# Kernel optimization log

Measured on AMD Instinct MI355X. Metric: run time of the kernel, lower is better.

Reference implementation:

```python
import math
import jax, jax.numpy as jnp
import numpy as np

NUM_HEADS = 8

def setup_inputs() -> dict:
    key = jax.random.key(0)
    ks = jax.random.split(key, 4)
    b, c, T, H, W = 8, 512, 8, 16, 16
    data_dim = T * H * W  # 2048
    x = jax.random.normal(ks[0], (b, c, T, H, W), dtype=jnp.float32)
    pos_emb = jax.random.normal(ks[1], (c, data_dim + 1), dtype=jnp.float32) / math.sqrt(c)
    w_qkv = jax.random.normal(ks[2], (3 * c, c), dtype=jnp.float32) * (1.0 / math.sqrt(c))
    b_qkv = jnp.zeros((3 * c,), dtype=jnp.float32)
    w_c = jax.random.normal(ks[3], (c, c), dtype=jnp.float32) * (1.0 / math.sqrt(c))
    b_c = jnp.zeros((c,), dtype=jnp.float32)
    return {"x": x, "pos_emb": pos_emb, "w_qkv": w_qkv, "b_qkv": b_qkv, "w_c": w_c, "b_c": b_c}

def reference(x, pos_emb, w_qkv, b_qkv, w_c, b_c):
    b, c = x.shape[0], x.shape[1]
    xf = x.reshape(b, c, -1)                                   # [b, c, THW]
    xf = jnp.concatenate([xf.mean(axis=-1, keepdims=True), xf], axis=-1)  # [b, c, T+1]
    xf = xf + pos_emb[None].astype(xf.dtype)
    qkv = jnp.einsum('oc,bct->bot', w_qkv, xf) + b_qkv[None, :, None]      # [b, 3c, L]
    L = qkv.shape[-1]
    ch = c // NUM_HEADS
    q, k, v = jnp.split(qkv, 3, axis=1)
    q = q.reshape(b * NUM_HEADS, ch, L)
    k = k.reshape(b * NUM_HEADS, ch, L)
    v = v.reshape(b * NUM_HEADS, ch, L)
    scale = 1.0 / math.sqrt(math.sqrt(ch))
    w = jnp.einsum('bct,bcs->bts', q * scale, k * scale)        # [bH, L, L]
    w = jax.nn.softmax(w.astype(jnp.float32), axis=-1).astype(qkv.dtype)
    a = jnp.einsum('bts,bcs->bct', w, v).reshape(b, c, L)       # [b, c, L]
    out = jnp.einsum('oc,bct->bot', w_c, a) + b_c[None, :, None]
    return out[:, :, 0]                                         # [b, out_dim]
```

## Files before the change

### kernel.cpp

```cpp
#include <hip/hip_runtime.h>

#define B 8
#define C 512
#define D 2048
#define L 2049
#define NH 8
#define CH 64
#define NLT 32
#define TLD 513

__device__ __forceinline__ float wave_sum(float v) {
  #pragma unroll
  for (int off = 32; off; off >>= 1) v += __shfl_down(v, off);
  return v;
}
__device__ __forceinline__ float wave_max(float v) {
  #pragma unroll
  for (int off = 32; off; off >>= 1) v = fmaxf(v, __shfl_down(v, off));
  return v;
}
__device__ __forceinline__ float lane_bcast(float v, int l) {
  return __uint_as_float(__builtin_amdgcn_readlane(__float_as_uint(v), l));
}

__global__ void __launch_bounds__(256) k_mean(const float* __restrict__ x, float* __restrict__ mean) {
  int row = blockIdx.x;
  const float4* xr = reinterpret_cast<const float4*>(x + (size_t)row * D);
  float s = 0.f;
  #pragma unroll
  for (int i = 0; i < 2; ++i) {
    float4 v = xr[threadIdx.x + i * 256];
    s += (v.x + v.y) + (v.z + v.w);
  }
  __shared__ float red[4];
  s = wave_sum(s);
  if ((threadIdx.x & 63) == 0) red[threadIdx.x >> 6] = s;
  __syncthreads();
  if (threadIdx.x == 0) mean[row] = (red[0] + red[1] + red[2] + red[3]) * (1.0f / D);
}

__global__ void __launch_bounds__(256) k_qu(const float* __restrict__ wqkv,
                                            const float* __restrict__ bqkv,
                                            const float* __restrict__ pos,
                                            const float* __restrict__ mean,
                                            float* __restrict__ u,
                                            float* __restrict__ logit0,
                                            float* __restrict__ mps_g) {
  int bh = blockIdx.x, b = bh >> 3, h = bh & 7;
  int tid = threadIdx.x, wid = tid >> 6, lane = tid & 63;
  __shared__ float mps[C];
  __shared__ float q0s[CH];
  __shared__ float us[C];
  __shared__ float red[4];
  for (int c = tid; c < C; c += 256) {
    float v = mean[b * C + c] + pos[(size_t)c * L];
    mps[c] = v;
    if (h == 0) mps_g[b * C + c] = v;
  }
  __syncthreads();
  for (int j = wid; j < CH; j += 4) {
    const float* wr = wqkv + (size_t)(h * CH + j) * C;
    float acc = 0.f;
    #pragma unroll
    for (int k = 0; k < 8; ++k) acc += wr[lane + k * 64] * mps[lane + k * 64];
    acc = wave_sum(acc);
    if (lane == 0) q0s[j] = acc + bqkv[h * CH + j];
  }
  __syncthreads();
  float a0 = 0.f, a1 = 0.f;
  #pragma unroll 4
  for (int j = 0; j < CH; ++j) {
    float qv = q0s[j];
    const float* wkr = wqkv + (size_t)(C + h * CH + j) * C;
    a0 += qv * wkr[tid];
    a1 += qv * wkr[tid + 256];
  }
  a0 *= 0.125f; a1 *= 0.125f;
  us[tid] = a0; us[tid + 256] = a1;
  u[(size_t)bh * C + tid] = a0;
  u[(size_t)bh * C + tid + 256] = a1;
  __syncthreads();
  float p = us[tid] * mps[tid] + us[tid + 256] * mps[tid + 256];
  p = wave_sum(p);
  if (lane == 0) red[wid] = p;
  __syncthreads();
  if (tid == 0) logit0[bh] = red[0] + red[1] + red[2] + red[3];
}

__global__ void __launch_bounds__(512, 1) k_fused_lx(
    const float* __restrict__ x, const float* __restrict__ pos,
    const float* __restrict__ u_g,
    float* __restrict__ xpart, float* __restrict__ mpart, float* __restrict__ spart) {
  __shared__ float tile[64][TLD];
  __shared__ float rlds[8][NH][64];
  __shared__ float e_t[64][9];
  int lt = blockIdx.x, b = blockIdx.y;
  int tid = threadIdx.x, wid = tid >> 6, lane = tid & 63;
  int cg = wid * 64;
  int col = lt * 64 + lane;

  float ureg[NH];
  #pragma unroll
  for (int h = 0; h < NH; ++h) ureg[h] = u_g[(size_t)(b * NH + h) * C + cg + lane];

  float acc[NH];
  #pragma unroll
  for (int h = 0; h < NH; ++h) acc[h] = 0.f;

  const float* xp = x + ((size_t)(b * C + cg)) * D + col;
  const float* pp = pos + (size_t)cg * L + col + 1;
  #pragma unroll
  for (int cc = 0; cc < 64; ++cc) {
    float v = xp[(size_t)cc * D] + pp[(size_t)cc * L];
    tile[lane][cg + cc] = v;
    #pragma unroll
    for (int h = 0; h < NH; ++h) acc[h] += lane_bcast(ureg[h], cc) * v;
  }
  #pragma unroll
  for (int h = 0; h < NH; ++h) rlds[wid][h][lane] = acc[h];
  __syncthreads();

  {
    int h = wid;
    float lg = 0.f;
    #pragma unroll
    for (int w = 0; w < 8; ++w) lg += rlds[w][h][lane];
    float m = wave_max(lg);
    m = lane_bcast(m, 0);
    float e = __expf(lg - m);
    float s = wave_sum(e);
    e_t[lane][h] = e;
    if (lane == 0) {
      mpart[(b * NH + h) * NLT + lt] = m;
      spart[(b * NH + h) * NLT + lt] = s;
    }
  }
  __syncthreads();

  float epre[NH];
  #pragma unroll
  for (int h = 0; h < NH; ++h) epre[h] = e_t[lane][h];
  float a2[NH];
  #pragma unroll
  for (int h = 0; h < NH; ++h) a2[h] = 0.f;
  #pragma unroll
  for (int l = 0; l < 64; ++l) {
    float xv = tile[l][tid];
    #pragma unroll
    for (int h = 0; h < NH; ++h) a2[h] += lane_bcast(epre[h], l) * xv;
  }
  #pragma unroll
  for (int h = 0; h < NH; ++h)
    xpart[(((size_t)b * NLT + lt) * NH + h) * C + tid] = a2[h];
}

__global__ void __launch_bounds__(512) k_a0(
    const float* __restrict__ xpart, const float* __restrict__ mpart,
    const float* __restrict__ spart, const float* __restrict__ logit0,
    const float* __restrict__ mps_g,
    const float* __restrict__ wqkv, const float* __restrict__ bqkv,
    float* __restrict__ a0v) {
  int bh = blockIdx.x, b = bh >> 3, h = bh & 7;
  int tid = threadIdx.x, wid = tid >> 6, lane = tid & 63;
  __shared__ float row[C];
  float lg0 = logit0[bh];
  float mt = (lane < NLT) ? mpart[bh * NLT + lane] : -3.0e38f;
  float M = fmaxf(lane_bcast(wave_max(mt), 0), lg0);
  float rr = (lane < NLT) ? __expf(mt - M) : 0.f;
  float st = (lane < NLT) ? spart[bh * NLT + lane] * rr : 0.f;
  float S = lane_bcast(wave_sum(st), 0) + __expf(lg0 - M);
  float Sinv = 1.0f / S;
  float acc = 0.f;
  #pragma unroll
  for (int t = 0; t < NLT; ++t)
    acc += xpart[(((size_t)b * NLT + t) * NH + h) * C + tid] * lane_bcast(rr, t);
  acc = (acc + __expf(lg0 - M) * mps_g[b * C + tid]) * Sinv;
  row[tid] = acc;
  __syncthreads();
  float xr[8];
  #pragma unroll
  for (int k = 0; k < 8; ++k) xr[k] = row[k * 64 + lane];
  #pragma unroll 2
  for (int j = 0; j < 8; ++j) {
    int o = h * CH + wid * 8 + j;
    const float* wr = wqkv + (size_t)(2 * C + o) * C;
    float d = 0.f;
    #pragma unroll
    for (int k = 0; k < 8; ++k) d += wr[k * 64 + lane] * xr[k];
    d = wave_sum(d);
    if (lane == 0) a0v[b * C + o] = d + bqkv[2 * C + o];
  }
}

__global__ void __launch_bounds__(512) k_out(const float* __restrict__ wc,
                                             const float* __restrict__ bc,
                                             const float* __restrict__ a0v,
                                             float* __restrict__ out) {
  int bid = blockIdx.x, b = bid >> 3, og = (bid & 7) * 64;
  int tid = threadIdx.x, wid = tid >> 6, lane = tid & 63;
  __shared__ float row[C];
  row[tid] = a0v[b * C + tid];
  __syncthreads();
  float xr[8];
  #pragma unroll
  for (int k = 0; k < 8; ++k) xr[k] = row[k * 64 + lane];
  #pragma unroll 2
  for (int j = 0; j < 8; ++j) {
    int o = og + wid * 8 + j;
    const float* wr = wc + (size_t)o * C;
    float d = 0.f;
    #pragma unroll
    for (int k = 0; k < 8; ++k) d += wr[k * 64 + lane] * xr[k];
    d = wave_sum(d);
    if (lane == 0) out[b * C + o] = d + bc[o];
  }
}

extern "C" void kernel_launch(void* const* d_in, const int* in_sizes, int n_in,
                              void* d_out, int out_size, void* d_ws, size_t ws_size,
                              hipStream_t stream) {
  const float* x    = (const float*)d_in[0];
  const float* pos  = (const float*)d_in[1];
  const float* wqkv = (const float*)d_in[2];
  const float* bqkv = (const float*)d_in[3];
  const float* wc   = (const float*)d_in[4];
  const float* bc   = (const float*)d_in[5];
  float* out = (float*)d_out;
  float* ws  = (float*)d_ws;

  float* mean   = ws;
  float* u      = ws + 4096;
  float* logit0 = ws + 36864;
  float* mpart  = ws + 36928;
  float* spart  = ws + 38976;
  float* a0v    = ws + 41024;
  float* mps_g  = ws + 45120;
  float* xpart  = ws + 49216;

  hipLaunchKernelGGL(k_mean,     dim3(B * C),    dim3(256), 0, stream, x, mean);
  hipLaunchKernelGGL(k_qu,       dim3(B * NH),   dim3(256), 0, stream, wqkv, bqkv, pos, mean, u, logit0, mps_g);
  hipLaunchKernelGGL(k_fused_lx, dim3(NLT, B),   dim3(512), 0, stream, x, pos, u, xpart, mpart, spart);
  hipLaunchKernelGGL(k_a0,       dim3(B * NH),   dim3(512), 0, stream, xpart, mpart, spart, logit0,
                     mps_g, wqkv, bqkv, a0v);
  hipLaunchKernelGGL(k_out,      dim3(B * NH),   dim3(512), 0, stream, wc, bc, a0v, out);
}
```

Before: 56.03 us.

## Fuse value and output projections into one tail kernel and batch loads in main kernel

Folds the pos-embedding add into the mean kernel, and merges the softmax combine, value projection and output projection into a single per-batch tail kernel, removing one launch and an intermediate buffer. In the main fused kernel, all 64 x and pos loads are issued up front into a register array, and the second phase reads the LDS tile in batches of 32, to expose more memory-level parallelism. Launch bounds are raised to allow two blocks per CU. The tail kernel runs only 8 blocks and streams both weight matrices serially per block, so it may become latency-bound, and the large register arrays under a tighter register budget risk spills.

```diff
diff --git a/kernel.cpp b/kernel.cpp
--- a/kernel.cpp
+++ b/kernel.cpp
@@ -23,7 +23,9 @@
   return __uint_as_float(__builtin_amdgcn_readlane(__float_as_uint(v), l));
 }
 
-__global__ void __launch_bounds__(256) k_mean(const float* __restrict__ x, float* __restrict__ mean) {
+__global__ void __launch_bounds__(256) k_mean(const float* __restrict__ x,
+                                              const float* __restrict__ pos,
+                                              float* __restrict__ mps_g) {
   int row = blockIdx.x;
   const float4* xr = reinterpret_cast<const float4*>(x + (size_t)row * D);
   float s = 0.f;
@@ -36,27 +38,23 @@
   s = wave_sum(s);
   if ((threadIdx.x & 63) == 0) red[threadIdx.x >> 6] = s;
   __syncthreads();
-  if (threadIdx.x == 0) mean[row] = (red[0] + red[1] + red[2] + red[3]) * (1.0f / D);
+  if (threadIdx.x == 0)
+    mps_g[row] = (red[0] + red[1] + red[2] + red[3]) * (1.0f / D)
+               + pos[(size_t)(row & (C - 1)) * L];
 }
 
 __global__ void __launch_bounds__(256) k_qu(const float* __restrict__ wqkv,
                                             const float* __restrict__ bqkv,
-                                            const float* __restrict__ pos,
-                                            const float* __restrict__ mean,
+                                            const float* __restrict__ mps_g,
                                             float* __restrict__ u,
-                                            float* __restrict__ logit0,
-                                            float* __restrict__ mps_g) {
+                                            float* __restrict__ logit0) {
   int bh = blockIdx.x, b = bh >> 3, h = bh & 7;
   int tid = threadIdx.x, wid = tid >> 6, lane = tid & 63;
   __shared__ float mps[C];
   __shared__ float q0s[CH];
   __shared__ float us[C];
   __shared__ float red[4];
-  for (int c = tid; c < C; c += 256) {
-    float v = mean[b * C + c] + pos[(size_t)c * L];
-    mps[c] = v;
-    if (h == 0) mps_g[b * C + c] = v;
-  }
+  for (int c = tid; c < C; c += 256) mps[c] = mps_g[b * C + c];
   __syncthreads();
   for (int j = wid; j < CH; j += 4) {
     const float* wr = wqkv + (size_t)(h * CH + j) * C;
@@ -87,7 +85,7 @@
   if (tid == 0) logit0[bh] = red[0] + red[1] + red[2] + red[3];
 }
 
-__global__ void __launch_bounds__(512, 1) k_fused_lx(
+__global__ void __launch_bounds__(512, 2) k_fused_lx(
     const float* __restrict__ x, const float* __restrict__ pos,
     const float* __restrict__ u_g,
     float* __restrict__ xpart, float* __restrict__ mpart, float* __restrict__ spart) {
@@ -103,18 +101,23 @@
   #pragma unroll
   for (int h = 0; h < NH; ++h) ureg[h] = u_g[(size_t)(b * NH + h) * C + cg + lane];
 
-  float acc[NH];
-  #pragma unroll
-  for (int h = 0; h < NH; ++h) acc[h] = 0.f;
-
   const float* xp = x + ((size_t)(b * C + cg)) * D + col;
   const float* pp = pos + (size_t)cg * L + col + 1;
+
+  float v_arr[64];
+  #pragma unroll
+  for (int cc = 0; cc < 64; ++cc) v_arr[cc] = xp[(size_t)cc * D];
+  #pragma unroll
+  for (int cc = 0; cc < 64; ++cc) v_arr[cc] += pp[(size_t)cc * L];
+
+  float acc[NH];
+  #pragma unroll
+  for (int h = 0; h < NH; ++h) acc[h] = 0.f;
   #pragma unroll
   for (int cc = 0; cc < 64; ++cc) {
-    float v = xp[(size_t)cc * D] + pp[(size_t)cc * L];
-    tile[lane][cg + cc] = v;
-    #pragma unroll
-    for (int h = 0; h < NH; ++h) acc[h] += lane_bcast(ureg[h], cc) * v;
+    tile[lane][cg + cc] = v_arr[cc];
+    #pragma unroll
+    for (int h = 0; h < NH; ++h) acc[h] += lane_bcast(ureg[h], cc) * v_arr[cc];
   }
   #pragma unroll
   for (int h = 0; h < NH; ++h) rlds[wid][h][lane] = acc[h];
@@ -144,75 +147,85 @@
   #pragma unroll
   for (int h = 0; h < NH; ++h) a2[h] = 0.f;
   #pragma unroll
-  for (int l = 0; l < 64; ++l) {
-    float xv = tile[l][tid];
-    #pragma unroll
-    for (int h = 0; h < NH; ++h) a2[h] += lane_bcast(epre[h], l) * xv;
+  for (int half = 0; half < 2; ++half) {
+    float xv[32];
+    #pragma unroll
+    for (int i = 0; i < 32; ++i) xv[i] = tile[half * 32 + i][tid];
+    #pragma unroll
+    for (int i = 0; i < 32; ++i) {
+      #pragma unroll
+      for (int h = 0; h < NH; ++h)
+        a2[h] += lane_bcast(epre[h], half * 32 + i) * xv[i];
+    }
   }
   #pragma unroll
   for (int h = 0; h < NH; ++h)
     xpart[(((size_t)b * NLT + lt) * NH + h) * C + tid] = a2[h];
 }
 
-__global__ void __launch_bounds__(512) k_a0(
+__global__ void __launch_bounds__(512) k_tail(
     const float* __restrict__ xpart, const float* __restrict__ mpart,
     const float* __restrict__ spart, const float* __restrict__ logit0,
     const float* __restrict__ mps_g,
     const float* __restrict__ wqkv, const float* __restrict__ bqkv,
-    float* __restrict__ a0v) {
-  int bh = blockIdx.x, b = bh >> 3, h = bh & 7;
+    const float* __restrict__ wc, const float* __restrict__ bc,
+    float* __restrict__ out) {
+  int b = blockIdx.x;
   int tid = threadIdx.x, wid = tid >> 6, lane = tid & 63;
-  __shared__ float row[C];
-  float lg0 = logit0[bh];
-  float mt = (lane < NLT) ? mpart[bh * NLT + lane] : -3.0e38f;
-  float M = fmaxf(lane_bcast(wave_max(mt), 0), lg0);
-  float rr = (lane < NLT) ? __expf(mt - M) : 0.f;
-  float st = (lane < NLT) ? spart[bh * NLT + lane] * rr : 0.f;
-  float S = lane_bcast(wave_sum(st), 0) + __expf(lg0 - M);
-  float Sinv = 1.0f / S;
-  float acc = 0.f;
-  #pragma unroll
-  for (int t = 0; t < NLT; ++t)
-    acc += xpart[(((size_t)b * NLT + t) * NH + h) * C + tid] * lane_bcast(rr, t);
-  acc = (acc + __expf(lg0 - M) * mps_g[b * C + tid]) * Sinv;
-  row[tid] = acc;
-  __syncthreads();
-  float xr[8];
-  #pragma unroll
-  for (int k = 0; k < 8; ++k) xr[k] = row[k * 64 + lane];
-  #pragma unroll 2
-  for (int j = 0; j < 8; ++j) {
-    int o = h * CH + wid * 8 + j;
-    const float* wr = wqkv + (size_t)(2 * C + o) * C;
-    float d = 0.f;
-    #pragma unroll
-    for (int k = 0; k < 8; ++k) d += wr[k * 64 + lane] * xr[k];
-    d = wave_sum(d);
-    if (lane == 0) a0v[b * C + o] = d + bqkv[2 * C + o];
-  }
-}
-
-__global__ void __launch_bounds__(512) k_out(const float* __restrict__ wc,
-                                             const float* __restrict__ bc,
-                                             const float* __restrict__ a0v,
-                                             float* __restrict__ out) {
-  int bid = blockIdx.x, b = bid >> 3, og = (bid & 7) * 64;
-  int tid = threadIdx.x, wid = tid >> 6, lane = tid & 63;
-  __shared__ float row[C];
-  row[tid] = a0v[b * C + tid];
-  __syncthreads();
-  float xr[8];
-  #pragma unroll
-  for (int k = 0; k < 8; ++k) xr[k] = row[k * 64 + lane];
-  #pragma unroll 2
-  for (int j = 0; j < 8; ++j) {
-    int o = og + wid * 8 + j;
-    const float* wr = wc + (size_t)o * C;
-    float d = 0.f;
-    #pragma unroll
-    for (int k = 0; k < 8; ++k) d += wr[k * 64 + lane] * xr[k];
-    d = wave_sum(d);
-    if (lane == 0) out[b * C + o] = d + bc[o];
+  __shared__ float xb[NH][C];
+  __shared__ float a0s[C];
+
+  {
+    int h = wid, bh = b * NH + h;
+    float lg0 = logit0[bh];
+    float mt = (lane < NLT) ? mpart[bh * NLT + lane] : -3.0e38f;
+    float M = fmaxf(lane_bcast(wave_max(mt), 0), lg0);
+    float rr = (lane < NLT) ? __expf(mt - M) : 0.f;
+    float st = (lane < NLT) ? spart[bh * NLT + lane] * rr : 0.f;
+    float S = lane_bcast(wave_sum(st), 0) + __expf(lg0 - M);
+    float Sinv = 1.0f / S;
+    float e0 = __expf(lg0 - M);
+    #pragma unroll
+    for (int kb = 0; kb < 8; ++kb) {
+      int c = kb * 64 + lane;
+      float acc = 0.f;
+      #pragma unroll
+      for (int t = 0; t < NLT; ++t)
+        acc += xpart[(((size_t)b * NLT + t) * NH + h) * C + c] * lane_bcast(rr, t);
+      xb[h][c] = (acc + e0 * mps_g[b * C + c]) * Sinv;
+    }
+  }
+  __syncthreads();
+
+  {
+    float xr[8];
+    #pragma unroll
+    for (int k = 0; k < 8; ++k) xr[k] = xb[wid][k * 64 + lane];
+    for (int j = 0; j < 64; ++j) {
+      int o = wid * 64 + j;
+      const float* wr = wqkv + (size_t)(2 * C + o) * C;
+      float d = 0.f;
+      #pragma unroll
+      for (int k = 0; k < 8; ++k) d += wr[k * 64 + lane] * xr[k];
+      d = wave_sum(d);
+      if (lane == 0) a0s[o] = d + bqkv[2 * C + o];
+    }
+  }
+  __syncthreads();
+
+  {
+    float ar[8];
+    #pragma unroll
+    for (int k = 0; k < 8; ++k) ar[k] = a0s[k * 64 + lane];
+    for (int j = 0; j < 64; ++j) {
+      int o = wid * 64 + j;
+      const float* wr = wc + (size_t)o * C;
+      float d = 0.f;
+      #pragma unroll
+      for (int k = 0; k < 8; ++k) d += wr[k * 64 + lane] * ar[k];
+      d = wave_sum(d);
+      if (lane == 0) out[b * C + o] = d + bc[o];
+    }
   }
 }
 
@@ -228,19 +241,16 @@
   float* out = (float*)d_out;
   float* ws  = (float*)d_ws;
 
-  float* mean   = ws;
+  float* mps_g  = ws;
   float* u      = ws + 4096;
   float* logit0 = ws + 36864;
   float* mpart  = ws + 36928;
   float* spart  = ws + 38976;
-  float* a0v    = ws + 41024;
-  float* mps_g  = ws + 45120;
-  float* xpart  = ws + 49216;
-
-  hipLaunchKernelGGL(k_mean,     dim3(B * C),    dim3(256), 0, stream, x, mean);
-  hipLaunchKernelGGL(k_qu,       dim3(B * NH),   dim3(256), 0, stream, wqkv, bqkv, pos, mean, u, logit0, mps_g);
-  hipLaunchKernelGGL(k_fused_lx, dim3(NLT, B),   dim3(512), 0, stream, x, pos, u, xpart, mpart, spart);
-  hipLaunchKernelGGL(k_a0,       dim3(B * NH),   dim3(512), 0, stream, xpart, mpart, spart, logit0,
-                     mps_g, wqkv, bqkv, a0v);
-  hipLaunchKernelGGL(k_out,      dim3(B * NH),   dim3(512), 0, stream, wc, bc, a0v, out);
-}
+  float* xpart  = ws + 41024;
+
+  hipLaunchKernelGGL(k_mean,     dim3(B * C),  dim3(256), 0, stream, x, pos, mps_g);
+  hipLaunchKernelGGL(k_qu,       dim3(B * NH), dim3(256), 0, stream, wqkv, bqkv, mps_g, u, logit0);
+  hipLaunchKernelGGL(k_fused_lx, dim3(NLT, B), dim3(512), 0, stream, x, pos, u, xpart, mpart, spart);
+  hipLaunchKernelGGL(k_tail,     dim3(B),      dim3(512), 0, stream, xpart, mpart, spart, logit0,
+                     mps_g, wqkv, bqkv, wc, bc, out);
+}
```

New measurement: 191.9 us. +242.6%, slower.
